# Optimization experiments

Hardware: AMD Instinct MI355X
Metric: run time of the kernel (lower is better)

Reference implementation:

```python
import jax, jax.numpy as jnp
import numpy as np

NUM_HEADS = 12
HEAD_DIM = 64
EPS = 1e-6


def rms_norm(x, w):
    # normalize over last dim (head_dim)
    norm = jax.lax.rsqrt(jnp.mean(x * x, axis=-1, keepdims=True) + EPS)
    return x * norm * w


def apply_rotary_emb(x, cos, sin):
    x1, x2 = jnp.split(x, 2, axis=-1)
    return jnp.concatenate([x1 * cos - x2 * sin, x2 * cos + x1 * sin], axis=-1)


def setup_inputs() -> dict:
    key = jax.random.key(0)
    ks = jax.random.split(key, 6)
    B, N, C = 4, 2048, 768
    return {
        "x": jax.random.normal(ks[0], (B, N, C), dtype=jnp.float32),
        "cos": jax.random.uniform(ks[1], (1, 1, N, HEAD_DIM // 2), dtype=jnp.float32),
        "sin": jax.random.uniform(ks[2], (1, 1, N, HEAD_DIM // 2), dtype=jnp.float32),
        "qkv_w": jax.random.normal(ks[3], (3 * C, C), dtype=jnp.float32) * (C ** -0.5),
        "q_norm_w": jnp.ones((HEAD_DIM,), dtype=jnp.float32),
        "k_norm_w": jnp.ones((HEAD_DIM,), dtype=jnp.float32),
        "proj_w": jax.random.normal(ks[4], (C, C), dtype=jnp.float32) * (C ** -0.5),
        "proj_b": jnp.zeros((C,), dtype=jnp.float32),
    }


def reference(x, cos, sin, qkv_w, q_norm_w, k_norm_w, proj_w, proj_b):
    B, N, C = x.shape
    H, D = NUM_HEADS, HEAD_DIM
    scale = D ** -0.5
    # qkv projection: [B,N,3C] -> [3,B,H,N,D]
    qkv = jnp.einsum('bnc,oc->bno', x, qkv_w)
    qkv = qkv.reshape(B, N, 3, H, D).transpose(2, 0, 3, 1, 4)
    q, k, v = qkv[0], qkv[1], qkv[2]
    q = rms_norm(q, q_norm_w)
    k = rms_norm(k, k_norm_w)
    q = apply_rotary_emb(q, cos, sin)
    k = apply_rotary_emb(k, cos, sin)
    attn = jnp.einsum('bhqd,bhkd->bhqk', q, k) * scale
    attn = jax.nn.softmax(attn, axis=-1)
    out = jnp.einsum('bhqk,bhkd->bhqd', attn, v)
    out = out.transpose(0, 2, 1, 3).reshape(B, N, C)
    out = jnp.einsum('bnc,oc->bno', out, proj_w) + proj_b
    return out
```

## Files before the change

kernel.cpp:

```cpp
#include <hip/hip_runtime.h>
#include <hip/hip_bf16.h>

#define BB 4
#define NN 2048
#define CC 768
#define HH 12
#define DD 64

typedef __bf16 bf16;
typedef __attribute__((ext_vector_type(8))) __bf16 bf16x8;
typedef __attribute__((ext_vector_type(4))) __bf16 bf16x4;
typedef __attribute__((ext_vector_type(4))) float f32x4;

#define SZ_X    (BB * NN * CC)
#define SZ_QKVW (3 * CC * CC)
#define SZ_PW   (CC * CC)
#define SZ_QKV  ((size_t)BB * NN * 3 * CC)

#define OFF_X    0
#define OFF_VT   0
#define OFF_QW   (OFF_X + SZ_X)
#define OFF_PW   (OFF_QW + SZ_QKVW)
#define OFF_QKV  (OFF_PW + SZ_PW)

__device__ __forceinline__ void async16(const bf16* g, bf16* l) {
    __builtin_amdgcn_global_load_lds(
        (const __attribute__((address_space(1))) unsigned int*)g,
        (__attribute__((address_space(3))) unsigned int*)l, 16, 0, 0);
}

__device__ __forceinline__ void cast8(const float* __restrict__ src,
                                      bf16* __restrict__ dst, int i) {
    f32x4 a = ((const f32x4*)src)[2 * i];
    f32x4 b = ((const f32x4*)src)[2 * i + 1];
    bf16x8 o;
#pragma unroll
    for (int j = 0; j < 4; ++j) { o[j] = (bf16)a[j]; o[j + 4] = (bf16)b[j]; }
    ((bf16x8*)dst)[i] = o;
}

__global__ __launch_bounds__(256) void convert3(
    const float* __restrict__ x, const float* __restrict__ qkvw,
    const float* __restrict__ pw, bf16* __restrict__ ws) {
    const int t = blockIdx.x * 256 + threadIdx.x;
    const int S = gridDim.x * 256;
    for (int i = t; i < SZ_X / 8;    i += S) cast8(x,    ws + OFF_X,  i);
    for (int i = t; i < SZ_QKVW / 8; i += S) cast8(qkvw, ws + OFF_QW, i);
    for (int i = t; i < SZ_PW / 8;   i += S) cast8(pw,   ws + OFF_PW, i);
}

template <bool HAS_BIAS, typename OutT>
__global__ __launch_bounds__(256) void gemm128(
    const bf16* __restrict__ A, int lda, const bf16* __restrict__ W,
    const float* __restrict__ bias, OutT* __restrict__ C,
    int M, int Nn, int K) {
    __shared__ __align__(16) bf16 As[128 * 64];
    __shared__ __align__(16) bf16 Bs[128 * 64];
    const int tid  = threadIdx.x;
    const int wave = tid >> 6;
    const int lane = tid & 63;
    const int quad = lane >> 4;
    const int l16  = lane & 15;
    const int m0 = blockIdx.y * 128;
    const int n0 = blockIdx.x * 128;
    const int wm = (wave >> 1) * 64;
    const int wn = (wave & 1) * 64;
    const int srow = lane >> 3;
    const int swz  = (lane & 7) ^ srow;

    f32x4 acc[4][4];
#pragma unroll
    for (int i = 0; i < 4; ++i)
#pragma unroll
        for (int j = 0; j < 4; ++j) acc[i][j] = (f32x4){0.f, 0.f, 0.f, 0.f};

    for (int k0 = 0; k0 < K; k0 += 64) {
#pragma unroll
        for (int i = 0; i < 4; ++i) {
            int row = i * 32 + wave * 8 + srow;
            async16(A + (size_t)(m0 + row) * lda + k0 + swz * 8,
                    &As[(i * 32 + wave * 8) * 64]);
            async16(W + (size_t)(n0 + row) * K + k0 + swz * 8,
                    &Bs[(i * 32 + wave * 8) * 64]);
        }
        __syncthreads();
#pragma unroll
        for (int kk = 0; kk < 2; ++kk) {
            const int slot = ((kk * 4 + quad) ^ (l16 & 7)) * 8;
            bf16x8 af[4], bf[4];
#pragma unroll
            for (int mt = 0; mt < 4; ++mt)
                af[mt] = *(const bf16x8*)(&As[(wm + mt * 16 + l16) * 64 + slot]);
#pragma unroll
            for (int nt = 0; nt < 4; ++nt)
                bf[nt] = *(const bf16x8*)(&Bs[(wn + nt * 16 + l16) * 64 + slot]);
#pragma unroll
            for (int mt = 0; mt < 4; ++mt)
#pragma unroll
                for (int nt = 0; nt < 4; ++nt)
                    acc[mt][nt] = __builtin_amdgcn_mfma_f32_16x16x32_bf16(
                        af[mt], bf[nt], acc[mt][nt], 0, 0, 0);
        }
        __syncthreads();
    }
#pragma unroll
    for (int mt = 0; mt < 4; ++mt)
#pragma unroll
        for (int nt = 0; nt < 4; ++nt)
#pragma unroll
            for (int r = 0; r < 4; ++r) {
                int row = m0 + wm + mt * 16 + quad * 4 + r;
                int col = n0 + wn + nt * 16 + l16;
                float v = acc[mt][nt][r];
                if (HAS_BIAS) v += bias[col];
                C[(size_t)row * Nn + col] = (OutT)v;
            }
}

__global__ __launch_bounds__(256) void transpose_v(
    const bf16* __restrict__ qkv, bf16* __restrict__ Vt) {
    __shared__ __align__(16) bf16 Ts[64 * 64];
    const int t = threadIdx.x;
    const int bh = blockIdx.x;
    const int kt = blockIdx.y;
    const int b = bh / HH, h = bh % HH;
    const size_t rs = 3 * CC;
    const bf16* src = qkv + (size_t)b * NN * rs + 2 * CC + h * DD;
    {
        const int keyl = t >> 2;
        const int d0   = (t & 3) * 16;
#pragma unroll
        for (int half = 0; half < 2; ++half) {
            int dd = d0 + half * 8;
            bf16x8 v = *(const bf16x8*)(src + (size_t)(kt * 64 + keyl) * rs + dd);
            int dc = dd >> 3;
            *(bf16x8*)(&Ts[keyl * 64 + ((dc ^ (keyl >> 3)) * 8)]) = v;
        }
    }
    __syncthreads();
#pragma unroll
    for (int p = 0; p < 2; ++p) {
        const int d  = p * 32 + (t >> 3);
        const int kc = (t & 7) * 8;
        bf16x8 v;
#pragma unroll
        for (int j = 0; j < 8; ++j) {
            int key = kc + j;
            v[j] = Ts[key * 64 + (((d >> 3) ^ (key >> 3)) * 8 + (d & 7))];
        }
        *(bf16x8*)(Vt + ((size_t)bh * DD + d) * NN + kt * 64 + kc) = v;
    }
}

__global__ __launch_bounds__(256) void norm_rope(
    bf16* __restrict__ qkv, const float* __restrict__ cosb,
    const float* __restrict__ sinb, const float* __restrict__ qw,
    const float* __restrict__ kw) {
    const int lane = threadIdx.x & 63;
    const int wave = threadIdx.x >> 6;
    const int job = blockIdx.x * 4 + wave;
    const int h = job % HH;
    const int s = (job / HH) % 2;
    const int g = job / (2 * HH);
    const int gr = lane >> 3;
    const int sl = lane & 7;
    const int bn = g * 8 + gr;
    const int n  = bn & (NN - 1);

    bf16* row = qkv + (size_t)bn * (3 * CC) + s * CC + h * DD + sl * 8;
    bf16x8 v = *(const bf16x8*)row;
    float x[8];
    float ss = 0.f;
#pragma unroll
    for (int j = 0; j < 8; ++j) { x[j] = (float)v[j]; ss += x[j] * x[j]; }
    ss += __shfl_xor(ss, 1, 64);
    ss += __shfl_xor(ss, 2, 64);
    ss += __shfl_xor(ss, 4, 64);
    float r = rsqrtf(ss * (1.0f / 64.0f) + 1e-6f);

    const float* wp = ((s == 0) ? qw : kw) + sl * 8;
    f32x4 w0 = *(const f32x4*)(wp);
    f32x4 w1 = *(const f32x4*)(wp + 4);
#pragma unroll
    for (int j = 0; j < 4; ++j) { x[j] *= r * w0[j]; x[j + 4] *= r * w1[j]; }

    float xp[8];
#pragma unroll
    for (int j = 0; j < 8; ++j) xp[j] = __shfl_xor(x[j], 4, 64);

    const int jb = (sl & 3) * 8;
    f32x4 c0 = *(const f32x4*)(cosb + n * 32 + jb);
    f32x4 c1 = *(const f32x4*)(cosb + n * 32 + jb + 4);
    f32x4 s0 = *(const f32x4*)(sinb + n * 32 + jb);
    f32x4 s1 = *(const f32x4*)(sinb + n * 32 + jb + 4);
    const float sgn = (sl < 4) ? -1.f : 1.f;
    float y[8];
#pragma unroll
    for (int j = 0; j < 4; ++j) {
        y[j]     = x[j]     * c0[j] + sgn * xp[j]     * s0[j];
        y[j + 4] = x[j + 4] * c1[j] + sgn * xp[j + 4] * s1[j];
    }
    const float qs = (s == 0) ? 0.18033688f : 1.0f;
    bf16x8 o;
#pragma unroll
    for (int j = 0; j < 8; ++j) o[j] = (bf16)(y[j] * qs);
    *(bf16x8*)row = o;
}

__global__ __launch_bounds__(256) void flash_attn(
    const bf16* __restrict__ qkv, const bf16* __restrict__ Vt,
    bf16* __restrict__ Oqkv) {
    __shared__ __align__(16) bf16 Ks[64 * 64];
    __shared__ __align__(16) bf16 Vs[64 * 64];
    __shared__ __align__(16) bf16 Ps[4][32 * 72];
    const int tid  = threadIdx.x;
    const int wave = tid >> 6;
    const int lane = tid & 63;
    const int quad = lane >> 4;
    const int l16  = lane & 15;
    const int r7   = l16 & 7;
    const int bh = blockIdx.x;
    const int qt = blockIdx.y;
    const int b = bh / HH, h = bh % HH;
    const size_t rs = 3 * CC;
    const bf16* Qb  = qkv + (size_t)b * NN * rs + h * DD;
    const bf16* Kb  = Qb + CC;
    const bf16* Vtb = Vt + (size_t)bh * DD * NN;

    bf16x8 qf[2][2];
#pragma unroll
    for (int f = 0; f < 2; ++f) {
        const int qrow = qt * 128 + wave * 32 + f * 16 + l16;
#pragma unroll
        for (int hf = 0; hf < 2; ++hf)
            qf[f][hf] = *(const bf16x8*)(Qb + (size_t)qrow * rs + hf * 32 + quad * 8);
    }

    f32x4 accO[2][4];
#pragma unroll
    for (int f = 0; f < 2; ++f)
#pragma unroll
        for (int i = 0; i < 4; ++i) accO[f][i] = (f32x4){0.f, 0.f, 0.f, 0.f};
    float lsum[2] = {0.f, 0.f};

    const int srow = lane >> 3;
    const int swz  = (lane & 7) ^ srow;

    for (int kt = 0; kt < NN / 64; ++kt) {
#pragma unroll
        for (int i = 0; i < 2; ++i) {
            int row = i * 32 + wave * 8 + srow;
            async16(Kb + (size_t)(kt * 64 + row) * rs + swz * 8,
                    &Ks[(i * 32 + wave * 8) * 64]);
            async16(Vtb + (size_t)row * NN + kt * 64 + swz * 8,
                    &Vs[(i * 32 + wave * 8) * 64]);
        }
        __syncthreads();

        f32x4 s[2][4];
#pragma unroll
        for (int nt = 0; nt < 4; ++nt) {
            const int row = nt * 16 + l16;
            bf16x8 kf0 = *(const bf16x8*)(&Ks[row * 64 + (quad ^ r7) * 8]);
            bf16x8 kf1 = *(const bf16x8*)(&Ks[row * 64 + ((quad + 4) ^ r7) * 8]);
#pragma unroll
            for (int f = 0; f < 2; ++f) {
                f32x4 z = (f32x4){0.f, 0.f, 0.f, 0.f};
                z = __builtin_amdgcn_mfma_f32_16x16x32_bf16(kf0, qf[f][0], z, 0, 0, 0);
                s[f][nt] = __builtin_amdgcn_mfma_f32_16x16x32_bf16(kf1, qf[f][1], z, 0, 0, 0);
            }
        }

#pragma unroll
        for (int f = 0; f < 2; ++f)
#pragma unroll
            for (int nt = 0; nt < 4; ++nt) {
                bf16x4 pk;
#pragma unroll
                for (int r = 0; r < 4; ++r) {
                    float pv = __builtin_amdgcn_exp2f(s[f][nt][r]);
                    lsum[f] += pv;
                    pk[r] = (bf16)pv;
                }
                *(bf16x4*)(&Ps[wave][(f * 16 + l16) * 72 + nt * 16 + quad * 4]) = pk;
            }
        __asm__ volatile("s_waitcnt lgkmcnt(0)" ::: "memory");

        bf16x8 pf0[2], pf1[2];
#pragma unroll
        for (int f = 0; f < 2; ++f) {
            pf0[f] = *(const bf16x8*)(&Ps[wave][(f * 16 + l16) * 72 + quad * 8]);
            pf1[f] = *(const bf16x8*)(&Ps[wave][(f * 16 + l16) * 72 + 32 + quad * 8]);
        }
#pragma unroll
        for (int nt = 0; nt < 4; ++nt) {
            const int rowd = nt * 16 + l16;
            bf16x8 vf0 = *(const bf16x8*)(&Vs[rowd * 64 + (quad ^ r7) * 8]);
            bf16x8 vf1 = *(const bf16x8*)(&Vs[rowd * 64 + ((quad + 4) ^ r7) * 8]);
#pragma unroll
            for (int f = 0; f < 2; ++f) {
                accO[f][nt] = __builtin_amdgcn_mfma_f32_16x16x32_bf16(pf0[f], vf0, accO[f][nt], 0, 0, 0);
                accO[f][nt] = __builtin_amdgcn_mfma_f32_16x16x32_bf16(pf1[f], vf1, accO[f][nt], 0, 0, 0);
            }
        }
        __syncthreads();
    }

#pragma unroll
    for (int f = 0; f < 2; ++f) {
        lsum[f] += __shfl_xor(lsum[f], 16, 64);
        lsum[f] += __shfl_xor(lsum[f], 32, 64);
    }

#pragma unroll
    for (int f = 0; f < 2; ++f)
#pragma unroll
        for (int r = 0; r < 4; ++r) {
            float inv = 1.0f / __shfl(lsum[f], quad * 4 + r, 64);
            int n = qt * 128 + wave * 32 + f * 16 + quad * 4 + r;
#pragma unroll
            for (int nt = 0; nt < 4; ++nt) {
                int col = h * DD + nt * 16 + l16;
                Oqkv[(size_t)(b * NN + n) * rs + 2 * CC + col] = (bf16)(accO[f][nt][r] * inv);
            }
        }
}

extern "C" void kernel_launch(void* const* d_in, const int* in_sizes, int n_in,
                              void* d_out, int out_size, void* d_ws, size_t ws_size,
                              hipStream_t stream) {
    const float* x     = (const float*)d_in[0];
    const float* cosb  = (const float*)d_in[1];
    const float* sinb  = (const float*)d_in[2];
    const float* qkv_w = (const float*)d_in[3];
    const float* qnw   = (const float*)d_in[4];
    const float* knw   = (const float*)d_in[5];
    const float* pw    = (const float*)d_in[6];
    const float* pb    = (const float*)d_in[7];
    float* out = (float*)d_out;

    bf16* ws  = (bf16*)d_ws;
    bf16* xb  = ws + OFF_X;
    bf16* vt  = ws + OFF_VT;
    bf16* qwb = ws + OFF_QW;
    bf16* pwb = ws + OFF_PW;
    bf16* qkv = ws + OFF_QKV;

    const int M = BB * NN;

    convert3<<<1024, 256, 0, stream>>>(x, qkv_w, pw, ws);

    dim3 g1(3 * CC / 128, M / 128);
    gemm128<false, bf16><<<g1, 256, 0, stream>>>(xb, CC, qwb, nullptr, qkv, M, 3 * CC, CC);

    dim3 g2(BB * HH, NN / 64);
    transpose_v<<<g2, 256, 0, stream>>>(qkv, vt);

    norm_rope<<<(2 * HH * (BB * NN / 8)) / 4, 256, 0, stream>>>(qkv, cosb, sinb, qnw, knw);

    dim3 g4(BB * HH, NN / 128);
    flash_attn<<<g4, 256, 0, stream>>>(qkv, vt, qkv);

    dim3 g5(CC / 128, M / 128);
    gemm128<true, float><<<g5, 256, 0, stream>>>(qkv + 2 * CC, 3 * CC, pwb, pb, out, M, CC, CC);
}
```

Before: 241.9 us.

## Fuse RMS norm and rotary embedding into QKV GEMM epilogue

Adds a dedicated QKV GEMM whose epilogue applies per-head RMS norm, rotary embedding and the query scale directly on the MFMA accumulators. Each wave tile covers exactly one 64-wide head, so the norm reduction uses cross-lane shuffles. The separate norm_rope kernel is removed, saving one launch plus a full read and write of the Q/K portion of the qkv buffer. The cost is a heavier epilogue with scalar bf16 stores and per-row cos/sin loads, which may raise register pressure in the GEMM.

```diff
diff --git a/kernel.cpp b/kernel.cpp
--- a/kernel.cpp
+++ b/kernel.cpp
@@ -47,6 +47,117 @@
     for (int i = t; i < SZ_X / 8;    i += S) cast8(x,    ws + OFF_X,  i);
     for (int i = t; i < SZ_QKVW / 8; i += S) cast8(qkvw, ws + OFF_QW, i);
     for (int i = t; i < SZ_PW / 8;   i += S) cast8(pw,   ws + OFF_PW, i);
+}
+
+__global__ __launch_bounds__(256) void gemm_qkv(
+    const bf16* __restrict__ A, const bf16* __restrict__ W,
+    bf16* __restrict__ C, const float* __restrict__ cosb,
+    const float* __restrict__ sinb, const float* __restrict__ qw,
+    const float* __restrict__ kw) {
+    __shared__ __align__(16) bf16 As[128 * 64];
+    __shared__ __align__(16) bf16 Bs[128 * 64];
+    const int tid  = threadIdx.x;
+    const int wave = tid >> 6;
+    const int lane = tid & 63;
+    const int quad = lane >> 4;
+    const int l16  = lane & 15;
+    const int m0 = blockIdx.y * 128;
+    const int n0 = blockIdx.x * 128;
+    const int wm = (wave >> 1) * 64;
+    const int wn = (wave & 1) * 64;
+    const int srow = lane >> 3;
+    const int swz  = (lane & 7) ^ srow;
+    const int K = CC;
+    const int Nn = 3 * CC;
+
+    f32x4 acc[4][4];
+#pragma unroll
+    for (int i = 0; i < 4; ++i)
+#pragma unroll
+        for (int j = 0; j < 4; ++j) acc[i][j] = (f32x4){0.f, 0.f, 0.f, 0.f};
+
+    for (int k0 = 0; k0 < K; k0 += 64) {
+#pragma unroll
+        for (int i = 0; i < 4; ++i) {
+            int row = i * 32 + wave * 8 + srow;
+            async16(A + (size_t)(m0 + row) * CC + k0 + swz * 8,
+                    &As[(i * 32 + wave * 8) * 64]);
+            async16(W + (size_t)(n0 + row) * K + k0 + swz * 8,
+                    &Bs[(i * 32 + wave * 8) * 64]);
+        }
+        __syncthreads();
+#pragma unroll
+        for (int kk = 0; kk < 2; ++kk) {
+            const int slot = ((kk * 4 + quad) ^ (l16 & 7)) * 8;
+            bf16x8 af[4], bf[4];
+#pragma unroll
+            for (int mt = 0; mt < 4; ++mt)
+                af[mt] = *(const bf16x8*)(&As[(wm + mt * 16 + l16) * 64 + slot]);
+#pragma unroll
+            for (int nt = 0; nt < 4; ++nt)
+                bf[nt] = *(const bf16x8*)(&Bs[(wn + nt * 16 + l16) * 64 + slot]);
+#pragma unroll
+            for (int mt = 0; mt < 4; ++mt)
+#pragma unroll
+                for (int nt = 0; nt < 4; ++nt)
+                    acc[mt][nt] = __builtin_amdgcn_mfma_f32_16x16x32_bf16(
+                        af[mt], bf[nt], acc[mt][nt], 0, 0, 0);
+        }
+        __syncthreads();
+    }
+
+    const int colblk = n0 + wn;
+    const int sector = colblk / CC;
+    if (sector == 2) {
+#pragma unroll
+        for (int mt = 0; mt < 4; ++mt)
+#pragma unroll
+            for (int nt = 0; nt < 4; ++nt)
+#pragma unroll
+                for (int r = 0; r < 4; ++r) {
+                    int row = m0 + wm + mt * 16 + quad * 4 + r;
+                    int col = colblk + nt * 16 + l16;
+                    C[(size_t)row * Nn + col] = (bf16)acc[mt][nt][r];
+                }
+    } else {
+        const float* wp = (sector == 0) ? qw : kw;
+        const float qs = (sector == 0) ? 0.18033688f : 1.0f;
+        float wv[4];
+#pragma unroll
+        for (int nt = 0; nt < 4; ++nt) wv[nt] = wp[nt * 16 + l16];
+#pragma unroll
+        for (int mt = 0; mt < 4; ++mt)
+#pragma unroll
+            for (int r = 0; r < 4; ++r) {
+                const int row = m0 + wm + mt * 16 + quad * 4 + r;
+                const int n   = row & (NN - 1);
+                float v[4];
+#pragma unroll
+                for (int nt = 0; nt < 4; ++nt) v[nt] = acc[mt][nt][r];
+                float ss = v[0] * v[0] + v[1] * v[1] + v[2] * v[2] + v[3] * v[3];
+                ss += __shfl_xor(ss, 1, 64);
+                ss += __shfl_xor(ss, 2, 64);
+                ss += __shfl_xor(ss, 4, 64);
+                ss += __shfl_xor(ss, 8, 64);
+                const float rn = rsqrtf(ss * (1.0f / 64.0f) + 1e-6f);
+#pragma unroll
+                for (int nt = 0; nt < 4; ++nt) v[nt] *= rn * wv[nt];
+                const float c0 = cosb[n * 32 + l16];
+                const float c1 = cosb[n * 32 + 16 + l16];
+                const float s0 = sinb[n * 32 + l16];
+                const float s1 = sinb[n * 32 + 16 + l16];
+                float y[4];
+                y[0] = v[0] * c0 - v[2] * s0;
+                y[1] = v[1] * c1 - v[3] * s1;
+                y[2] = v[2] * c0 + v[0] * s0;
+                y[3] = v[3] * c1 + v[1] * s1;
+#pragma unroll
+                for (int nt = 0; nt < 4; ++nt) {
+                    int col = colblk + nt * 16 + l16;
+                    C[(size_t)row * Nn + col] = (bf16)(y[nt] * qs);
+                }
+            }
+    }
 }
 
 template <bool HAS_BIAS, typename OutT>
@@ -150,61 +261,6 @@
         }
         *(bf16x8*)(Vt + ((size_t)bh * DD + d) * NN + kt * 64 + kc) = v;
     }
-}
-
-__global__ __launch_bounds__(256) void norm_rope(
-    bf16* __restrict__ qkv, const float* __restrict__ cosb,
-    const float* __restrict__ sinb, const float* __restrict__ qw,
-    const float* __restrict__ kw) {
-    const int lane = threadIdx.x & 63;
-    const int wave = threadIdx.x >> 6;
-    const int job = blockIdx.x * 4 + wave;
-    const int h = job % HH;
-    const int s = (job / HH) % 2;
-    const int g = job / (2 * HH);
-    const int gr = lane >> 3;
-    const int sl = lane & 7;
-    const int bn = g * 8 + gr;
-    const int n  = bn & (NN - 1);
-
-    bf16* row = qkv + (size_t)bn * (3 * CC) + s * CC + h * DD + sl * 8;
-    bf16x8 v = *(const bf16x8*)row;
-    float x[8];
-    float ss = 0.f;
-#pragma unroll
-    for (int j = 0; j < 8; ++j) { x[j] = (float)v[j]; ss += x[j] * x[j]; }
-    ss += __shfl_xor(ss, 1, 64);
-    ss += __shfl_xor(ss, 2, 64);
-    ss += __shfl_xor(ss, 4, 64);
-    float r = rsqrtf(ss * (1.0f / 64.0f) + 1e-6f);
-
-    const float* wp = ((s == 0) ? qw : kw) + sl * 8;
-    f32x4 w0 = *(const f32x4*)(wp);
-    f32x4 w1 = *(const f32x4*)(wp + 4);
-#pragma unroll
-    for (int j = 0; j < 4; ++j) { x[j] *= r * w0[j]; x[j + 4] *= r * w1[j]; }
-
-    float xp[8];
-#pragma unroll
-    for (int j = 0; j < 8; ++j) xp[j] = __shfl_xor(x[j], 4, 64);
-
-    const int jb = (sl & 3) * 8;
-    f32x4 c0 = *(const f32x4*)(cosb + n * 32 + jb);
-    f32x4 c1 = *(const f32x4*)(cosb + n * 32 + jb + 4);
-    f32x4 s0 = *(const f32x4*)(sinb + n * 32 + jb);
-    f32x4 s1 = *(const f32x4*)(sinb + n * 32 + jb + 4);
-    const float sgn = (sl < 4) ? -1.f : 1.f;
-    float y[8];
-#pragma unroll
-    for (int j = 0; j < 4; ++j) {
-        y[j]     = x[j]     * c0[j] + sgn * xp[j]     * s0[j];
-        y[j + 4] = x[j + 4] * c1[j] + sgn * xp[j + 4] * s1[j];
-    }
-    const float qs = (s == 0) ? 0.18033688f : 1.0f;
-    bf16x8 o;
-#pragma unroll
-    for (int j = 0; j < 8; ++j) o[j] = (bf16)(y[j] * qs);
-    *(bf16x8*)row = o;
 }
 
 __global__ __launch_bounds__(256) void flash_attn(
@@ -351,13 +407,11 @@
     convert3<<<1024, 256, 0, stream>>>(x, qkv_w, pw, ws);
 
     dim3 g1(3 * CC / 128, M / 128);
-    gemm128<false, bf16><<<g1, 256, 0, stream>>>(xb, CC, qwb, nullptr, qkv, M, 3 * CC, CC);
+    gemm_qkv<<<g1, 256, 0, stream>>>(xb, qwb, qkv, cosb, sinb, qnw, knw);
 
     dim3 g2(BB * HH, NN / 64);
     transpose_v<<<g2, 256, 0, stream>>>(qkv, vt);
 
-    norm_rope<<<(2 * HH * (BB * NN / 8)) / 4, 256, 0, stream>>>(qkv, cosb, sinb, qnw, knw);
-
     dim3 g4(BB * HH, NN / 128);
     flash_attn<<<g4, 256, 0, stream>>>(qkv, vt, qkv);
 
```

After: 240.8 us. Within noise of the previous version (-0.5%).
